# Performance work log

Hardware: AMD Instinct MI355X
Metric: run time of the kernel (lower is better)

## Reference

```python
import jax, jax.numpy as jnp
import numpy as np

QMIN = 0.0
QMAX = 255.0  # uint8, asymmetric


def fake_quant(x, scale, zp):
    # asymmetric uint8 fake-quantization: q = clamp(round(x/s + zp), 0, 255); dq = (q - zp) * s
    s = scale.reshape(())
    z = zp.reshape(())
    q = jnp.clip(jnp.round(x / s + z), QMIN, QMAX)
    return (q - z) * s


def setup_inputs() -> dict:
    key = jax.random.key(0)
    k1, k2 = jax.random.split(key)
    B, M, K, N = 4, 2048, 4096, 4096
    x1 = jax.random.normal(k1, (B, M, K), dtype=jnp.float32)
    x2 = jax.random.normal(k2, (B, K, N), dtype=jnp.float32)
    # realistic learned per-tensor scale / zero-point for ~N(0,1) data over uint8 range
    x1_scale = jnp.full((1,), 8.0 / 255.0, dtype=jnp.float32)
    x1_zp = jnp.full((1,), 128.0, dtype=jnp.float32)
    x2_scale = jnp.full((1,), 8.0 / 255.0, dtype=jnp.float32)
    x2_zp = jnp.full((1,), 128.0, dtype=jnp.float32)
    return {"x1": x1, "x2": x2, "x1_scale": x1_scale, "x1_zp": x1_zp,
            "x2_scale": x2_scale, "x2_zp": x2_zp}


def reference(x1, x2, x1_scale, x1_zp, x2_scale, x2_zp):
    q1 = fake_quant(x1, x1_scale, x1_zp)  # [B, M, K]
    q2 = fake_quant(x2, x2_scale, x2_zp)  # [B, K, N]
    return jnp.matmul(q1, q2)             # [B, M, N]
```

## Files before the change

### kernel.cpp

```cpp
#include <hip/hip_runtime.h>
#include <stdint.h>

typedef int v4i __attribute__((ext_vector_type(4)));

#define GLOBAL_AS __attribute__((address_space(1)))
#define LDS_AS __attribute__((address_space(3)))

__device__ __forceinline__ int quant1(float x, float s, float z, int zi) {
    float q = rintf(x / s + z);
    q = fminf(fmaxf(q, 0.0f), 255.0f);
    return (int)q - zi;
}

__device__ __forceinline__ unsigned qpack4(float4 v, float s, float z, int zi) {
    unsigned q0 = (unsigned)(quant1(v.x, s, z, zi) & 255);
    unsigned q1 = (unsigned)(quant1(v.y, s, z, zi) & 255);
    unsigned q2 = (unsigned)(quant1(v.z, s, z, zi) & 255);
    unsigned q3 = (unsigned)(quant1(v.w, s, z, zi) & 255);
    return q0 | (q1 << 8) | (q2 << 16) | (q3 << 24);
}

__global__ __launch_bounds__(256) void quant_lin(const float* __restrict__ x,
                                                 int8_t* __restrict__ out,
                                                 const float* __restrict__ sp,
                                                 const float* __restrict__ zp,
                                                 long n16) {
    float s = sp[0], z = zp[0];
    int zi = (int)rintf(z);
    long i = (long)blockIdx.x * 256 + threadIdx.x;
    if (i >= n16) return;
    const float4* xv = (const float4*)x;
    uint4 w;
    w.x = qpack4(xv[i * 4 + 0], s, z, zi);
    w.y = qpack4(xv[i * 4 + 1], s, z, zi);
    w.z = qpack4(xv[i * 4 + 2], s, z, zi);
    w.w = qpack4(xv[i * 4 + 3], s, z, zi);
    ((uint4*)out)[i] = w;
}

__global__ __launch_bounds__(256) void quant_bt(const float* __restrict__ x,
                                                int8_t* __restrict__ out,
                                                const float* __restrict__ sp,
                                                const float* __restrict__ zp) {
    constexpr int K = 4096, N = 4096;
    float s = sp[0], z = zp[0];
    int zi = (int)rintf(z);
    size_t bin = (size_t)blockIdx.z * K * N;
    int tid = threadIdx.x;
    int bk = tid >> 4;
    int bn = tid & 15;
    int k0 = blockIdx.y * 64, n0 = blockIdx.x * 64;
    __shared__ unsigned lds[64][17];
    unsigned o0 = 0, o1 = 0, o2 = 0, o3 = 0;
#pragma unroll
    for (int r = 0; r < 4; ++r) {
        float4 v = *(const float4*)(x + bin + (size_t)(k0 + bk * 4 + r) * N + n0 + bn * 4);
        o0 |= (unsigned)(quant1(v.x, s, z, zi) & 255) << (r * 8);
        o1 |= (unsigned)(quant1(v.y, s, z, zi) & 255) << (r * 8);
        o2 |= (unsigned)(quant1(v.z, s, z, zi) & 255) << (r * 8);
        o3 |= (unsigned)(quant1(v.w, s, z, zi) & 255) << (r * 8);
    }
    lds[bn * 4 + 0][bk] = o0;
    lds[bn * 4 + 1][bk] = o1;
    lds[bn * 4 + 2][bk] = o2;
    lds[bn * 4 + 3][bk] = o3;
    __syncthreads();
    int nl = tid >> 2, ch = tid & 3;
    uint4 w;
    w.x = lds[nl][ch * 4 + 0];
    w.y = lds[nl][ch * 4 + 1];
    w.z = lds[nl][ch * 4 + 2];
    w.w = lds[nl][ch * 4 + 3];
    *(uint4*)(out + bin + (size_t)(n0 + nl) * K + k0 + ch * 16) = w;
}

__global__ __launch_bounds__(512, 2) void gemm_i8(const int8_t* __restrict__ A,
                                                  const int8_t* __restrict__ Bt,
                                                  float* __restrict__ C,
                                                  const float* __restrict__ sp1,
                                                  const float* __restrict__ sp2) {
    constexpr int M = 2048, N = 4096, K = 4096;
    constexpr int BM = 256, BN = 256, BK = 128;
    constexpr int NT = K / BK;
    constexpr int NBN = N / BN;

    extern __shared__ char smem[];

    int b = blockIdx.z;
    const int8_t* Ab = A + (size_t)b * M * K;
    const int8_t* Bb = Bt + (size_t)b * N * K;
    float* Cb = C + (size_t)b * M * N;

    int nwg = gridDim.x;
    int wg = blockIdx.x;
    wg = (wg & 7) * (nwg >> 3) + (wg >> 3);
    int by = wg / NBN, bx = wg % NBN;
    int m0 = by * BM, n0 = bx * BN;

    int tid = threadIdx.x;
    int lane = tid & 63, wid = tid >> 6;
    int wr = wid >> 2, wc = wid & 3;
    int l15 = lane & 15, cb = lane >> 4;

    const int8_t* Abase = Ab + (size_t)m0 * K;
    const int8_t* Bbase = Bb + (size_t)n0 * K;

    int row0 = tid >> 2, cc0 = tid & 3;
    int sw0 = cc0 ^ ((row0 >> 1) & 3);
    const size_t JSTEP = (size_t)128 * K;
    const int8_t* pA0 = Abase + (size_t)row0 * K + sw0 * 16;
    const int8_t* pA1 = pA0 + 64;
    const int8_t* pB0 = Bbase + (size_t)row0 * K + sw0 * 16;
    const int8_t* pB1 = pB0 + 64;
    const unsigned dbase = (unsigned)tid * 16;

    int aoff[8], boff[4];
#pragma unroll
    for (int m = 0; m < 8; ++m) {
        int r = wr * 128 + m * 16 + l15;
        aoff[m] = r * 64 + ((cb ^ ((r >> 1) & 3)) * 16);
    }
#pragma unroll
    for (int n = 0; n < 4; ++n) {
        int r = wc * 64 + n * 16 + l15;
        boff[n] = r * 64 + ((cb ^ ((r >> 1) & 3)) * 16);
    }

    v4i zero = {0, 0, 0, 0};
    v4i acc[8][4];
#pragma unroll
    for (int m = 0; m < 8; ++m)
#pragma unroll
        for (int n = 0; n < 4; ++n) acc[m][n] = zero;

#define ISSUE(p, mat, kh, buf)                                                         \
    {                                                                                  \
        char* dst = smem + ((((buf)*2 + (mat)) * 2 + (kh)) * 16384) + dbase;           \
        __builtin_amdgcn_global_load_lds((const GLOBAL_AS void*)(p),                   \
                                         (LDS_AS void*)dst, 16, 0, 0);                 \
        __builtin_amdgcn_global_load_lds((const GLOBAL_AS void*)((p) + JSTEP),         \
                                         (LDS_AS void*)(dst + 8192), 16, 0, 0);        \
    }

#define LDA(Ar, h)                                                                     \
    _Pragma("unroll") for (int m = 0; m < 4; ++m)                                      \
        af[m] = *(const v4i*)((Ar) + aoff[(h)*4 + m]);

#define LDB(Br)                                                                        \
    _Pragma("unroll") for (int n = 0; n < 4; ++n)                                      \
        bf[n] = *(const v4i*)((Br) + boff[n]);

#define MM(mh)                                                                         \
    {                                                                                  \
        __builtin_amdgcn_s_setprio(1);                                                 \
        _Pragma("unroll") for (int m = 0; m < 4; ++m)                                  \
            _Pragma("unroll") for (int n = 0; n < 4; ++n)                              \
                acc[(mh)*4 + m][n] = __builtin_amdgcn_mfma_i32_16x16x64_i8(            \
                    af[m], bf[n], acc[(mh)*4 + m][n], 0, 0, 0);                        \
        __builtin_amdgcn_s_setprio(0);                                                 \
    }

    ISSUE(pA0, 0, 0, 0);
    ISSUE(pB0, 1, 0, 0);
    ISSUE(pA1, 0, 1, 0);
    ISSUE(pB1, 1, 1, 0);
    __syncthreads();

    for (int jt = 0; jt < NT; ++jt) {
        int buf = jt & 1;
        const char* Ar0 = smem + (buf * 4 + 0) * 16384;
        const char* Ar1 = smem + (buf * 4 + 1) * 16384;
        const char* Br0 = smem + (buf * 4 + 2) * 16384;
        const char* Br1 = smem + (buf * 4 + 3) * 16384;
        bool pf = (jt + 1 < NT);
        pA0 += BK; pA1 += BK; pB0 += BK; pB1 += BK;

        v4i af[4], bf[4];
        LDB(Br0);
        LDA(Ar0, 0);
        if (pf) ISSUE(pA0, 0, 0, buf ^ 1);
        MM(0);
        LDA(Ar0, 1);
        if (pf) ISSUE(pB0, 1, 0, buf ^ 1);
        MM(1);
        LDB(Br1);
        LDA(Ar1, 0);
        if (pf) ISSUE(pA1, 0, 1, buf ^ 1);
        MM(0);
        LDA(Ar1, 1);
        if (pf) ISSUE(pB1, 1, 1, buf ^ 1);
        MM(1);
        __syncthreads();
    }

    float sc = sp1[0] * sp2[0];
    int r0 = cb * 4;
#pragma unroll
    for (int m = 0; m < 8; ++m) {
#pragma unroll
        for (int n = 0; n < 4; ++n) {
            float* p = Cb + (size_t)(m0 + wr * 128 + m * 16 + r0) * N +
                       (n0 + wc * 64 + n * 16 + l15);
#pragma unroll
            for (int r = 0; r < 4; ++r) p[(size_t)r * N] = sc * (float)acc[m][n][r];
        }
    }
#undef ISSUE
#undef LDA
#undef LDB
#undef MM
}

extern "C" void kernel_launch(void* const* d_in, const int* in_sizes, int n_in,
                              void* d_out, int out_size, void* d_ws, size_t ws_size,
                              hipStream_t stream) {
    const float* x1 = (const float*)d_in[0];
    const float* x2 = (const float*)d_in[1];
    const float* s1 = (const float*)d_in[2];
    const float* z1 = (const float*)d_in[3];
    const float* s2 = (const float*)d_in[4];
    const float* z2 = (const float*)d_in[5];
    float* out = (float*)d_out;

    const int B = 4, M = 2048, K = 4096, N = 4096;
    const size_t ASZ = (size_t)B * M * K;
    const size_t BSZ = (size_t)B * K * N;
    dim3 blk(256);

    static int lds_attr_set = 0;
    if (!lds_attr_set) {
        (void)hipFuncSetAttribute((const void*)gemm_i8,
                                  hipFuncAttributeMaxDynamicSharedMemorySize, 131072);
        lds_attr_set = 1;
    }

    if (ws_size >= ASZ + BSZ) {
        int8_t* Aq = (int8_t*)d_ws;
        int8_t* Bq = Aq + ASZ;
        long n16 = (long)(ASZ / 16);
        quant_lin<<<dim3((unsigned)(n16 / 256)), blk, 0, stream>>>(x1, Aq, s1, z1, n16);
        quant_bt<<<dim3(N / 64, K / 64, B), blk, 0, stream>>>(x2, Bq, s2, z2);
        gemm_i8<<<dim3((M / 256) * (N / 256), 1, B), dim3(512), 131072, stream>>>(
            Aq, Bq, out, s1, s2);
    } else {
        const size_t AB = (size_t)M * K, BB = (size_t)K * N;
        int8_t* Aq = (int8_t*)d_ws;
        int8_t* Bq = Aq + AB;
        for (int b = 0; b < B; ++b) {
            long n16 = (long)(AB / 16);
            quant_lin<<<dim3((unsigned)(n16 / 256)), blk, 0, stream>>>(x1 + (size_t)b * AB, Aq, s1, z1, n16);
            quant_bt<<<dim3(N / 64, K / 64, 1), blk, 0, stream>>>(x2 + (size_t)b * BB, Bq, s2, z2);
            gemm_i8<<<dim3((M / 256) * (N / 256), 1, 1), dim3(512), 131072, stream>>>(
                Aq, Bq, out + (size_t)b * M * N, s1, s2);
        }
    }
}
```

Baseline: 262.8 us.

## Switch int8 GEMM to 32x32x32 MFMA with finer barrier-synchronized pipeline

Replaces the 16x16x64 int8 MFMA tiling with 32x32x32 i8 MFMA tiles (v16i accumulators) and rewrites the LDS fragment offsets and epilogue to match. It also swaps the per-iteration __syncthreads for explicit s_barrier plus vmcnt/lgkmcnt waits around each MFMA phase, so the async global-to-LDS prefetch overlaps compute more tightly. Larger MFMA tiles halve the LDS fragment reads per flop, but the extra barriers may add stalls, and the manual waitcnt logic risks correctness if the counts are wrong.

Result: no change. 266.7 us (+1.5%).

```diff
diff --git a/kernel.cpp b/kernel.cpp
--- a/kernel.cpp
+++ b/kernel.cpp
@@ -2,6 +2,7 @@
 #include <stdint.h>
 
 typedef int v4i __attribute__((ext_vector_type(4)));
+typedef int v16i __attribute__((ext_vector_type(16)));
 
 #define GLOBAL_AS __attribute__((address_space(1)))
 #define LDS_AS __attribute__((address_space(3)))
@@ -100,7 +101,7 @@
     int tid = threadIdx.x;
     int lane = tid & 63, wid = tid >> 6;
     int wr = wid >> 2, wc = wid & 3;
-    int l15 = lane & 15, cb = lane >> 4;
+    int l31 = lane & 31, hi = lane >> 5;
 
     const int8_t* Abase = Ab + (size_t)m0 * K;
     const int8_t* Bbase = Bb + (size_t)n0 * K;
@@ -114,24 +115,29 @@
     const int8_t* pB1 = pB0 + 64;
     const unsigned dbase = (unsigned)tid * 16;
 
-    int aoff[8], boff[4];
-#pragma unroll
-    for (int m = 0; m < 8; ++m) {
-        int r = wr * 128 + m * 16 + l15;
-        aoff[m] = r * 64 + ((cb ^ ((r >> 1) & 3)) * 16);
-    }
-#pragma unroll
-    for (int n = 0; n < 4; ++n) {
-        int r = wc * 64 + n * 16 + l15;
-        boff[n] = r * 64 + ((cb ^ ((r >> 1) & 3)) * 16);
-    }
-
-    v4i zero = {0, 0, 0, 0};
-    v4i acc[8][4];
-#pragma unroll
-    for (int m = 0; m < 8; ++m)
-#pragma unroll
-        for (int n = 0; n < 4; ++n) acc[m][n] = zero;
+    int aoff[4][2], boff[2][2];
+#pragma unroll
+    for (int m = 0; m < 4; ++m) {
+        int r = wr * 128 + m * 32 + l31;
+#pragma unroll
+        for (int j = 0; j < 2; ++j)
+            aoff[m][j] = r * 64 + (((j * 2 + hi) ^ ((r >> 1) & 3)) * 16);
+    }
+#pragma unroll
+    for (int n = 0; n < 2; ++n) {
+        int r = wc * 64 + n * 32 + l31;
+#pragma unroll
+        for (int j = 0; j < 2; ++j)
+            boff[n][j] = r * 64 + (((j * 2 + hi) ^ ((r >> 1) & 3)) * 16);
+    }
+
+    v16i acc[4][2];
+#pragma unroll
+    for (int m = 0; m < 4; ++m)
+#pragma unroll
+        for (int n = 0; n < 2; ++n)
+#pragma unroll
+            for (int e = 0; e < 16; ++e) acc[m][n][e] = 0;
 
 #define ISSUE(p, mat, kh, buf)                                                         \
     {                                                                                  \
@@ -142,29 +148,28 @@
                                          (LDS_AS void*)(dst + 8192), 16, 0, 0);        \
     }
 
-#define LDA(Ar, h)                                                                     \
-    _Pragma("unroll") for (int m = 0; m < 4; ++m)                                      \
-        af[m] = *(const v4i*)((Ar) + aoff[(h)*4 + m]);
-
-#define LDB(Br)                                                                        \
-    _Pragma("unroll") for (int n = 0; n < 4; ++n)                                      \
-        bf[n] = *(const v4i*)((Br) + boff[n]);
-
-#define MM(mh)                                                                         \
+#define MFMA8(mh)                                                                      \
     {                                                                                  \
         __builtin_amdgcn_s_setprio(1);                                                 \
-        _Pragma("unroll") for (int m = 0; m < 4; ++m)                                  \
-            _Pragma("unroll") for (int n = 0; n < 4; ++n)                              \
-                acc[(mh)*4 + m][n] = __builtin_amdgcn_mfma_i32_16x16x64_i8(            \
-                    af[m], bf[n], acc[(mh)*4 + m][n], 0, 0, 0);                        \
+        _Pragma("unroll") for (int m = 0; m < 2; ++m)                                  \
+            _Pragma("unroll") for (int n = 0; n < 2; ++n)                              \
+                _Pragma("unroll") for (int j = 0; j < 2; ++j)                          \
+                    acc[(mh)*2 + m][n] = __builtin_amdgcn_mfma_i32_32x32x32_i8(        \
+                        af[m][j], bf[n][j], acc[(mh)*2 + m][n], 0, 0, 0);              \
         __builtin_amdgcn_s_setprio(0);                                                 \
     }
+
+#define BAR_PRE()                                                                      \
+    __builtin_amdgcn_s_barrier();                                                      \
+    asm volatile("s_waitcnt lgkmcnt(0)" ::: "memory");                                 \
+    __builtin_amdgcn_sched_barrier(0);
 
     ISSUE(pA0, 0, 0, 0);
     ISSUE(pB0, 1, 0, 0);
     ISSUE(pA1, 0, 1, 0);
     ISSUE(pB1, 1, 1, 0);
-    __syncthreads();
+    asm volatile("s_waitcnt vmcnt(4)" ::: "memory");
+    __builtin_amdgcn_s_barrier();
 
     for (int jt = 0; jt < NT; ++jt) {
         int buf = jt & 1;
@@ -175,40 +180,72 @@
         bool pf = (jt + 1 < NT);
         pA0 += BK; pA1 += BK; pB0 += BK; pB1 += BK;
 
-        v4i af[4], bf[4];
-        LDB(Br0);
-        LDA(Ar0, 0);
+        v4i af[2][2], bf[2][2];
+#pragma unroll
+        for (int n = 0; n < 2; ++n)
+#pragma unroll
+            for (int j = 0; j < 2; ++j) bf[n][j] = *(const v4i*)(Br0 + boff[n][j]);
+#pragma unroll
+        for (int m = 0; m < 2; ++m)
+#pragma unroll
+            for (int j = 0; j < 2; ++j) af[m][j] = *(const v4i*)(Ar0 + aoff[m][j]);
         if (pf) ISSUE(pA0, 0, 0, buf ^ 1);
-        MM(0);
-        LDA(Ar0, 1);
+        BAR_PRE();
+        MFMA8(0);
+        __builtin_amdgcn_s_barrier();
+
+#pragma unroll
+        for (int m = 0; m < 2; ++m)
+#pragma unroll
+            for (int j = 0; j < 2; ++j) af[m][j] = *(const v4i*)(Ar0 + aoff[2 + m][j]);
         if (pf) ISSUE(pB0, 1, 0, buf ^ 1);
-        MM(1);
-        LDB(Br1);
-        LDA(Ar1, 0);
+        BAR_PRE();
+        MFMA8(1);
+        if (pf) asm volatile("s_waitcnt vmcnt(4)" ::: "memory");
+        else    asm volatile("s_waitcnt vmcnt(0)" ::: "memory");
+        __builtin_amdgcn_s_barrier();
+
+#pragma unroll
+        for (int n = 0; n < 2; ++n)
+#pragma unroll
+            for (int j = 0; j < 2; ++j) bf[n][j] = *(const v4i*)(Br1 + boff[n][j]);
+#pragma unroll
+        for (int m = 0; m < 2; ++m)
+#pragma unroll
+            for (int j = 0; j < 2; ++j) af[m][j] = *(const v4i*)(Ar1 + aoff[m][j]);
         if (pf) ISSUE(pA1, 0, 1, buf ^ 1);
-        MM(0);
-        LDA(Ar1, 1);
+        BAR_PRE();
+        MFMA8(0);
+        __builtin_amdgcn_s_barrier();
+
+#pragma unroll
+        for (int m = 0; m < 2; ++m)
+#pragma unroll
+            for (int j = 0; j < 2; ++j) af[m][j] = *(const v4i*)(Ar1 + aoff[2 + m][j]);
         if (pf) ISSUE(pB1, 1, 1, buf ^ 1);
-        MM(1);
-        __syncthreads();
+        BAR_PRE();
+        MFMA8(1);
+        if (pf) asm volatile("s_waitcnt vmcnt(4)" ::: "memory");
+        __builtin_amdgcn_s_barrier();
     }
 
     float sc = sp1[0] * sp2[0];
-    int r0 = cb * 4;
-#pragma unroll
-    for (int m = 0; m < 8; ++m) {
-#pragma unroll
-        for (int n = 0; n < 4; ++n) {
-            float* p = Cb + (size_t)(m0 + wr * 128 + m * 16 + r0) * N +
-                       (n0 + wc * 64 + n * 16 + l15);
-#pragma unroll
-            for (int r = 0; r < 4; ++r) p[(size_t)r * N] = sc * (float)acc[m][n][r];
+#pragma unroll
+    for (int mt = 0; mt < 4; ++mt) {
+#pragma unroll
+        for (int n = 0; n < 2; ++n) {
+            float* pc = Cb + (size_t)(m0 + wr * 128 + mt * 32 + 4 * hi) * N +
+                        (n0 + wc * 64 + n * 32 + l31);
+#pragma unroll
+            for (int g = 0; g < 4; ++g)
+#pragma unroll
+                for (int r = 0; r < 4; ++r)
+                    pc[(size_t)(g * 8 + r) * N] = sc * (float)acc[mt][n][g * 4 + r];
         }
     }
 #undef ISSUE
-#undef LDA
-#undef LDB
-#undef MM
+#undef MFMA8
+#undef BAR_PRE
 }
 
 extern "C" void kernel_launch(void* const* d_in, const int* in_sizes, int n_in,
```

## Restructure int8 GEMM main loop into half-tile stages with partial vmcnt waits

Applied to the files above, without the earlier changes.

Restructures the int8 MFMA main loop into two half-K stages per tile. Each stage loads all 8 A fragments and 4 B fragments, issues the next prefetch, then runs 32 MFMAs. Full __syncthreads are replaced with explicit lgkmcnt/vmcnt(4) waits plus s_barrier, so only the older half-tile loads must land before the next stage proceeds. The last iteration is peeled to drop the prefetch branch. The cost is more live fragment registers and a more fragile manual wait-count scheme.

Result: faster. 251.5 us (-4.3%).

```diff
diff --git a/kernel.cpp b/kernel.cpp
--- a/kernel.cpp
+++ b/kernel.cpp
@@ -142,55 +142,52 @@
                                          (LDS_AS void*)(dst + 8192), 16, 0, 0);        \
     }
 
-#define LDA(Ar, h)                                                                     \
-    _Pragma("unroll") for (int m = 0; m < 4; ++m)                                      \
-        af[m] = *(const v4i*)((Ar) + aoff[(h)*4 + m]);
-
-#define LDB(Br)                                                                        \
-    _Pragma("unroll") for (int n = 0; n < 4; ++n)                                      \
-        bf[n] = *(const v4i*)((Br) + boff[n]);
-
-#define MM(mh)                                                                         \
+#define HALF(Ar, Br, DOISSUE, NWAIT)                                                   \
     {                                                                                  \
+        v4i af[8], bf[4];                                                              \
+        _Pragma("unroll") for (int n = 0; n < 4; ++n)                                  \
+            bf[n] = *(const v4i*)((Br) + boff[n]);                                     \
+        _Pragma("unroll") for (int m = 0; m < 8; ++m)                                  \
+            af[m] = *(const v4i*)((Ar) + aoff[m]);                                     \
+        DOISSUE;                                                                       \
         __builtin_amdgcn_s_setprio(1);                                                 \
-        _Pragma("unroll") for (int m = 0; m < 4; ++m)                                  \
+        _Pragma("unroll") for (int m = 0; m < 8; ++m)                                  \
             _Pragma("unroll") for (int n = 0; n < 4; ++n)                              \
-                acc[(mh)*4 + m][n] = __builtin_amdgcn_mfma_i32_16x16x64_i8(            \
-                    af[m], bf[n], acc[(mh)*4 + m][n], 0, 0, 0);                        \
+                acc[m][n] = __builtin_amdgcn_mfma_i32_16x16x64_i8(af[m], bf[n],        \
+                                                                  acc[m][n], 0, 0, 0); \
         __builtin_amdgcn_s_setprio(0);                                                 \
+        asm volatile("s_waitcnt lgkmcnt(0)\n\ts_waitcnt vmcnt(" #NWAIT ")" ::: "memory"); \
+        __builtin_amdgcn_s_barrier();                                                  \
+        asm volatile("" ::: "memory");                                                 \
     }
 
     ISSUE(pA0, 0, 0, 0);
     ISSUE(pB0, 1, 0, 0);
     ISSUE(pA1, 0, 1, 0);
     ISSUE(pB1, 1, 1, 0);
-    __syncthreads();
-
-    for (int jt = 0; jt < NT; ++jt) {
+    asm volatile("s_waitcnt vmcnt(4)" ::: "memory");
+    __builtin_amdgcn_s_barrier();
+    asm volatile("" ::: "memory");
+
+    for (int jt = 0; jt < NT - 1; ++jt) {
         int buf = jt & 1;
         const char* Ar0 = smem + (buf * 4 + 0) * 16384;
         const char* Ar1 = smem + (buf * 4 + 1) * 16384;
         const char* Br0 = smem + (buf * 4 + 2) * 16384;
         const char* Br1 = smem + (buf * 4 + 3) * 16384;
-        bool pf = (jt + 1 < NT);
         pA0 += BK; pA1 += BK; pB0 += BK; pB1 += BK;
 
-        v4i af[4], bf[4];
-        LDB(Br0);
-        LDA(Ar0, 0);
-        if (pf) ISSUE(pA0, 0, 0, buf ^ 1);
-        MM(0);
-        LDA(Ar0, 1);
-        if (pf) ISSUE(pB0, 1, 0, buf ^ 1);
-        MM(1);
-        LDB(Br1);
-        LDA(Ar1, 0);
-        if (pf) ISSUE(pA1, 0, 1, buf ^ 1);
-        MM(0);
-        LDA(Ar1, 1);
-        if (pf) ISSUE(pB1, 1, 1, buf ^ 1);
-        MM(1);
-        __syncthreads();
+        HALF(Ar0, Br0, ISSUE(pA0, 0, 0, buf ^ 1); ISSUE(pB0, 1, 0, buf ^ 1), 4)
+        HALF(Ar1, Br1, ISSUE(pA1, 0, 1, buf ^ 1); ISSUE(pB1, 1, 1, buf ^ 1), 4)
+    }
+    {
+        int buf = (NT - 1) & 1;
+        const char* Ar0 = smem + (buf * 4 + 0) * 16384;
+        const char* Ar1 = smem + (buf * 4 + 1) * 16384;
+        const char* Br0 = smem + (buf * 4 + 2) * 16384;
+        const char* Br1 = smem + (buf * 4 + 3) * 16384;
+        HALF(Ar0, Br0, , 0)
+        HALF(Ar1, Br1, , 0)
     }
 
     float sc = sp1[0] * sp2[0];
@@ -206,9 +203,7 @@
         }
     }
 #undef ISSUE
-#undef LDA
-#undef LDB
-#undef MM
+#undef HALF
 }
 
 extern "C" void kernel_launch(void* const* d_in, const int* in_sizes, int n_in,
```
